# Performance work log

Hardware: AMD Instinct MI355X
Metric: run time of the kernel (lower is better)

Reference implementation:

```python
import math
import jax, jax.numpy as jnp
from jax import lax
import numpy as np

NUM_ANG_BINS = 8
NUM_SPATIAL_BINS = 4
SPATIAL_BIN_SIZE = 4
CLIPVAL = 0.2
STRIDE = 1
PAD = 1
EPS = 1e-10
DN = ('NCHW', 'OIHW', 'NCHW')


def _sift_pooling_kernel(ksize: int) -> np.ndarray:
    ks_2 = float(ksize) / 2.0
    xc2 = ks_2 - np.abs(np.arange(ksize, dtype=np.float32) + 0.5 - ks_2)
    return np.outer(xc2, xc2) / ks_2 ** 2  # (ksize, ksize)


def _reshape_kernel(kd: int, ky: int, kx: int) -> np.ndarray:
    numel = kd * ky * kx
    return np.eye(numel, dtype=np.float32).reshape(numel, kd, ky, kx)


def setup_inputs() -> dict:
    key = jax.random.key(0)
    x = jax.random.uniform(key, (2, 1, 512, 512), dtype=jnp.float32)
    pool_kernel = jnp.asarray(_sift_pooling_kernel(SPATIAL_BIN_SIZE))[None, None]  # (1,1,4,4)
    reshape_kernel = jnp.asarray(
        _reshape_kernel(NUM_ANG_BINS, NUM_SPATIAL_BINS, NUM_SPATIAL_BINS))  # (128,8,4,4)
    return {"x": x, "pool_kernel": pool_kernel, "reshape_kernel": reshape_kernel}


def _l2norm_c(t):
    # F.normalize(t, p=2, dim=1)
    n = jnp.sqrt(jnp.sum(t * t, axis=1, keepdims=True))
    return t / jnp.maximum(n, 1e-12)


def reference(x, pool_kernel, reshape_kernel):
    nbins = NUM_ANG_BINS
    two_pi = 2.0 * math.pi
    # spatial_gradient(mode='diff', normalized=True): central diff / 2 with replicate pad
    xp = jnp.pad(x, ((0, 0), (0, 0), (1, 1), (1, 1)), mode='edge')
    gx = 0.5 * (xp[:, :, 1:-1, 2:] - xp[:, :, 1:-1, :-2])
    gy = 0.5 * (xp[:, :, 2:, 1:-1] - xp[:, :, :-2, 1:-1])
    mag = jnp.sqrt(gx * gx + gy * gy + EPS)
    ori = jnp.arctan2(gy, gx + EPS) + two_pi
    o_big = nbins * ori / two_pi
    bo0f = jnp.floor(o_big)
    wo1 = o_big - bo0f
    bo0 = (bo0f.astype(jnp.int32) % nbins)[:, 0]          # (B,H,W)
    bo1 = (bo0 + 1) % nbins
    w0 = ((1.0 - wo1) * mag)[:, 0]                        # (B,H,W)
    w1 = (wo1 * mag)[:, 0]
    # soft-bin the magnitude into angular channels (vectorized over bins)
    ang = (jax.nn.one_hot(bo0, nbins, axis=1, dtype=x.dtype) * w0[:, None] +
           jax.nn.one_hot(bo1, nbins, axis=1, dtype=x.dtype) * w1[:, None])  # (B,8,H,W)
    # depthwise triangular pooling, padding ksize//2 -> (B,8,H+1,W+1)
    p = SPATIAL_BIN_SIZE // 2
    dw = jnp.tile(pool_kernel, (nbins, 1, 1, 1))  # (8,1,4,4)
    pooled = lax.conv_general_dilated(ang, dw, (1, 1), ((p, p), (p, p)),
                                      dimension_numbers=DN, feature_group_count=nbins)
    # neigh2channels identity conv -> (B,128,H,W)
    out = lax.conv_general_dilated(pooled, reshape_kernel, (STRIDE, STRIDE),
                                   ((PAD, PAD), (PAD, PAD)), dimension_numbers=DN)
    out = jnp.clip(_l2norm_c(out), 0.0, CLIPVAL)
    out = _l2norm_c(out)
    # RootSIFT
    n1 = jnp.maximum(jnp.sum(jnp.abs(out), axis=1, keepdims=True), 1e-12)
    out = jnp.sqrt(out / n1 + EPS)
    return out
```

## Files before the change

### kernel.cpp

```cpp
#include <hip/hip_runtime.h>
#include <hip/hip_fp16.h>
#include <math.h>

#define TY 4
#define TX 64
#define AH (TY + 6)
#define AW (TX + 6)
#define PH (TY + 3)
#define PW (TX + 3)
#define H 512
#define W 512

#define ANGX_OFF 0
#define ANG_OFF  21440
#define POOL_OFF 21440
#define SMEM_BYTES 36448

__device__ __forceinline__ unsigned short f2h(float f) {
    return __half_as_ushort(__float2half(f));
}
__device__ __forceinline__ float h2f_lo(unsigned int u) {
    return __half2float(__ushort_as_half((unsigned short)(u & 0xffffu)));
}
__device__ __forceinline__ float h2f_hi(unsigned int u) {
    return __half2float(__ushort_as_half((unsigned short)(u >> 16)));
}

__global__ __launch_bounds__(256, 4) void sift_kernel(const float* __restrict__ x,
                                                      float* __restrict__ out) {
    __shared__ __align__(16) char smem[SMEM_BYTES];
    float4* s_angx = (float4*)(smem + ANGX_OFF);
    uint4*  s_ang  = (uint4*)(smem + ANG_OFF);
    float4* s_pool = (float4*)(smem + POOL_OFF);

    const int tid = threadIdx.x;
    const int x0 = blockIdx.x * TX;
    const int y0 = blockIdx.y * TY;
    const int b  = blockIdx.z;
    const float* __restrict__ xb = x + (size_t)b * H * W;

    const float K1[4] = {0.25f, 0.75f, 0.75f, 0.25f};

    for (int i = tid; i < AH * AW; i += 256) {
        int ay = i / AW, ax = i - ay * AW;
        int gy = y0 - 3 + ay, gx = x0 - 3 + ax;
        float w0 = 0.f, w1 = 0.f;
        int bin = 0;
        if (gy >= 0 && gy < H && gx >= 0 && gx < W) {
            int gxm = gx - 1 < 0 ? 0 : gx - 1;
            int gxp = gx + 1 > W - 1 ? W - 1 : gx + 1;
            int gym = gy - 1 < 0 ? 0 : gy - 1;
            int gyp = gy + 1 > H - 1 ? H - 1 : gy + 1;
            float gxv = 0.5f * (xb[gy * W + gxp] - xb[gy * W + gxm]);
            float gyv = 0.5f * (xb[gyp * W + gx] - xb[gym * W + gx]);
            float mag = sqrtf(gxv * gxv + gyv * gyv + 1e-10f);
            float ori = atan2f(gyv, gxv + 1e-10f) + 6.283185307179586f;
            float obig = ori * 1.2732395447351628f;
            float bof = floorf(obig);
            float wo1 = obig - bof;
            bin = ((int)bof) & 7;
            w0 = (1.f - wo1) * mag;
            w1 = wo1 * mag;
        }
        unsigned short h0 = f2h(w0), h1 = f2h(w1);
        unsigned int pack01 = (unsigned int)h0 | ((unsigned int)h1 << 16);
        unsigned int ph0 = (unsigned int)h0 << 16;
        unsigned int pl1 = (unsigned int)h1;
        int j0 = bin >> 1;
        int j1 = ((bin + 1) & 7) >> 1;
        bool ev = (bin & 1) == 0;
        uint4 d;
        d.x = ev ? (j0 == 0 ? pack01 : 0u) : ((j0 == 0 ? ph0 : 0u) | (j1 == 0 ? pl1 : 0u));
        d.y = ev ? (j0 == 1 ? pack01 : 0u) : ((j0 == 1 ? ph0 : 0u) | (j1 == 1 ? pl1 : 0u));
        d.z = ev ? (j0 == 2 ? pack01 : 0u) : ((j0 == 2 ? ph0 : 0u) | (j1 == 2 ? pl1 : 0u));
        d.w = ev ? (j0 == 3 ? pack01 : 0u) : ((j0 == 3 ? ph0 : 0u) | (j1 == 3 ? pl1 : 0u));
        s_ang[i] = d;
    }
    __syncthreads();

    for (int i = tid; i < AH * PW; i += 256) {
        int ay = i / PW, pxl = i - ay * PW;
        float acc[8] = {0.f, 0.f, 0.f, 0.f, 0.f, 0.f, 0.f, 0.f};
        int base = ay * AW + pxl;
        #pragma unroll
        for (int v = 0; v < 4; ++v) {
            uint4 q = s_ang[base + v];
            float k = K1[v];
            acc[0] = fmaf(k, h2f_lo(q.x), acc[0]);
            acc[1] = fmaf(k, h2f_hi(q.x), acc[1]);
            acc[2] = fmaf(k, h2f_lo(q.y), acc[2]);
            acc[3] = fmaf(k, h2f_hi(q.y), acc[3]);
            acc[4] = fmaf(k, h2f_lo(q.z), acc[4]);
            acc[5] = fmaf(k, h2f_hi(q.z), acc[5]);
            acc[6] = fmaf(k, h2f_lo(q.w), acc[6]);
            acc[7] = fmaf(k, h2f_hi(q.w), acc[7]);
        }
        s_angx[(ay * 2 + 0) * PW + pxl] = make_float4(acc[0], acc[1], acc[2], acc[3]);
        s_angx[(ay * 2 + 1) * PW + pxl] = make_float4(acc[4], acc[5], acc[6], acc[7]);
    }
    __syncthreads();

    for (int i = tid; i < PH * PW * 2; i += 256) {
        int row = i / PW, pxl = i - row * PW;
        int pyl = row >> 1, dh = row & 1;
        float4 s = make_float4(0.f, 0.f, 0.f, 0.f);
        #pragma unroll
        for (int u = 0; u < 4; ++u) {
            float4 a = s_angx[((pyl + u) * 2 + dh) * PW + pxl];
            float k = K1[u];
            s.x = fmaf(k, a.x, s.x);
            s.y = fmaf(k, a.y, s.y);
            s.z = fmaf(k, a.z, s.z);
            s.w = fmaf(k, a.w, s.w);
        }
        bool valid = ((unsigned)(y0 - 1 + pyl) <= 512u) && ((unsigned)(x0 - 1 + pxl) <= 512u);
        if (!valid) s = make_float4(0.f, 0.f, 0.f, 0.f);
        s_pool[row * PW + pxl] = s;
    }
    __syncthreads();

    const int w  = tid >> 6;
    const int l  = tid & 63;
    const int dh = l >> 5;
    const int tx = 32 * (w & 1) + (l & 31);
    const int xx = x0 + tx;

    #pragma unroll
    for (int pp = 0; pp < 2; ++pp) {
        const int ty = 2 * pp + (w >> 1);
        const int yy = y0 + ty;
        float4 r[16];
        float ssq = 0.f;
        #pragma unroll
        for (int ky = 0; ky < 4; ++ky) {
            #pragma unroll
            for (int kx = 0; kx < 4; ++kx) {
                float4 t = s_pool[((ty + ky) * 2 + dh) * PW + (tx + kx)];
                r[ky * 4 + kx] = t;
                ssq = fmaf(t.x, t.x, ssq);
                ssq = fmaf(t.y, t.y, ssq);
                ssq = fmaf(t.z, t.z, ssq);
                ssq = fmaf(t.w, t.w, ssq);
            }
        }
        ssq += __shfl_xor(ssq, 32, 64);
        float inv = 1.f / fmaxf(sqrtf(ssq), 1e-12f);
        float su = 0.f;
        #pragma unroll
        for (int m = 0; m < 16; ++m) {
            float4 t = r[m];
            t.x = fminf(t.x * inv, 0.2f);
            t.y = fminf(t.y * inv, 0.2f);
            t.z = fminf(t.z * inv, 0.2f);
            t.w = fminf(t.w * inv, 0.2f);
            r[m] = t;
            su += (t.x + t.y) + (t.z + t.w);
        }
        su += __shfl_xor(su, 32, 64);
        float rs = 1.f / fmaxf(su, 1e-12f);
        float* __restrict__ op = out + ((size_t)b * 128 + dh * 64) * (size_t)(H * W)
                                     + (size_t)yy * W + xx;
        #pragma unroll
        for (int dd = 0; dd < 4; ++dd) {
            #pragma unroll
            for (int m = 0; m < 16; ++m) {
                float4 t = r[m];
                float comp = (dd == 0) ? t.x : (dd == 1) ? t.y : (dd == 2) ? t.z : t.w;
                float val = sqrtf(fmaf(comp, rs, 1e-10f));
                __builtin_nontemporal_store(val, op + (size_t)(dd * 16 + m) * (H * W));
            }
        }
    }
}

extern "C" void kernel_launch(void* const* d_in, const int* in_sizes, int n_in,
                              void* d_out, int out_size, void* d_ws, size_t ws_size,
                              hipStream_t stream) {
    const float* x = (const float*)d_in[0];
    float* out = (float*)d_out;
    const int B = in_sizes[0] / (H * W);
    dim3 grid(W / TX, H / TY, B);
    dim3 block(256);
    hipLaunchKernelGGL(sift_kernel, grid, block, 0, stream, x, out);
    (void)n_in; (void)out_size; (void)d_ws; (void)ws_size;
}
```

Before: 58.78 us.

## Compute two adjacent pixels per thread with 8-byte stores and fast math

Shared-memory pooled data is re-laid out as float2 per channel pair. Each thread now handles two horizontally adjacent pixels, reusing the overlapping 4x5 window, and writes float2 non-temporal stores. Per-pixel reductions now run across four lanes via shuffles. atan2 is replaced with a polynomial approximation that directly yields the bin coordinate, and sqrt, rcp and rsq use hardware intrinsics. This reduces store instruction count and transcendental cost, at the price of approximation error in orientation and normalization.

```diff
diff --git a/kernel.cpp b/kernel.cpp
--- a/kernel.cpp
+++ b/kernel.cpp
@@ -10,12 +10,15 @@
 #define PW (TX + 3)
 #define H 512
 #define W 512
+#define HW (H * W)
 
 #define ANGX_OFF 0
 #define ANG_OFF  21440
 #define POOL_OFF 21440
 #define SMEM_BYTES 36448
 
+typedef float f32x2 __attribute__((ext_vector_type(2)));
+
 __device__ __forceinline__ unsigned short f2h(float f) {
     return __half_as_ushort(__float2half(f));
 }
@@ -29,15 +32,16 @@
 __global__ __launch_bounds__(256, 4) void sift_kernel(const float* __restrict__ x,
                                                       float* __restrict__ out) {
     __shared__ __align__(16) char smem[SMEM_BYTES];
-    float4* s_angx = (float4*)(smem + ANGX_OFF);
-    uint4*  s_ang  = (uint4*)(smem + ANG_OFF);
-    float4* s_pool = (float4*)(smem + POOL_OFF);
+    float2* s_angx2 = (float2*)(smem + ANGX_OFF);
+    uint4*  s_ang   = (uint4*)(smem + ANG_OFF);
+    float2* s_pool2 = (float2*)(smem + POOL_OFF);
+    float*  s_poolf = (float*)(smem + POOL_OFF);
 
     const int tid = threadIdx.x;
     const int x0 = blockIdx.x * TX;
     const int y0 = blockIdx.y * TY;
     const int b  = blockIdx.z;
-    const float* __restrict__ xb = x + (size_t)b * H * W;
+    const float* __restrict__ xb = x + (size_t)b * HW;
 
     const float K1[4] = {0.25f, 0.75f, 0.75f, 0.25f};
 
@@ -48,17 +52,26 @@
         int bin = 0;
         if (gy >= 0 && gy < H && gx >= 0 && gx < W) {
             int gxm = gx - 1 < 0 ? 0 : gx - 1;
-            int gxp = gx + 1 > W - 1 ? W - 1 : gx + 1;
+            int gxp_ = gx + 1 > W - 1 ? W - 1 : gx + 1;
             int gym = gy - 1 < 0 ? 0 : gy - 1;
-            int gyp = gy + 1 > H - 1 ? H - 1 : gy + 1;
-            float gxv = 0.5f * (xb[gy * W + gxp] - xb[gy * W + gxm]);
-            float gyv = 0.5f * (xb[gyp * W + gx] - xb[gym * W + gx]);
-            float mag = sqrtf(gxv * gxv + gyv * gyv + 1e-10f);
-            float ori = atan2f(gyv, gxv + 1e-10f) + 6.283185307179586f;
-            float obig = ori * 1.2732395447351628f;
-            float bof = floorf(obig);
-            float wo1 = obig - bof;
-            bin = ((int)bof) & 7;
+            int gyp_ = gy + 1 > H - 1 ? H - 1 : gy + 1;
+            float gxv = 0.5f * (xb[gy * W + gxp_] - xb[gy * W + gxm]);
+            float gyv = 0.5f * (xb[gyp_ * W + gx] - xb[gym * W + gx]);
+            float mag = __builtin_amdgcn_sqrtf(gxv * gxv + gyv * gyv + 1e-10f);
+            float gxe = gxv + 1e-10f;
+            float axv = fabsf(gxe), ayv = fabsf(gyv);
+            float mn = fminf(axv, ayv), mx = fmaxf(axv, ayv);
+            float t = mn * __builtin_amdgcn_rcpf(fmaxf(mx, 1e-30f));
+            float t2 = t * t;
+            float p = t * fmaf(t2, fmaf(t2, fmaf(t2, fmaf(t2,
+                        fmaf(t2, -0.01492385f, 0.06704027f),
+                        -0.14824684f), 0.2464268f), -0.4235113f), 1.2732106f);
+            float q = (ayv > axv) ? (2.0f - p) : p;
+            q = (gxe < 0.0f) ? (4.0f - q) : q;
+            float o = (gyv < 0.0f) ? (0.0f - q) : q;
+            float of = floorf(o);
+            float wo1 = o - of;
+            bin = ((int)of) & 7;
             w0 = (1.f - wo1) * mag;
             w1 = wo1 * mag;
         }
@@ -95,79 +108,105 @@
             acc[6] = fmaf(k, h2f_lo(q.w), acc[6]);
             acc[7] = fmaf(k, h2f_hi(q.w), acc[7]);
         }
-        s_angx[(ay * 2 + 0) * PW + pxl] = make_float4(acc[0], acc[1], acc[2], acc[3]);
-        s_angx[(ay * 2 + 1) * PW + pxl] = make_float4(acc[4], acc[5], acc[6], acc[7]);
+        #pragma unroll
+        for (int g = 0; g < 4; ++g)
+            s_angx2[(ay * 4 + g) * PW + pxl] = make_float2(acc[2 * g], acc[2 * g + 1]);
     }
     __syncthreads();
 
-    for (int i = tid; i < PH * PW * 2; i += 256) {
+    for (int i = tid; i < PH * 4 * PW; i += 256) {
         int row = i / PW, pxl = i - row * PW;
-        int pyl = row >> 1, dh = row & 1;
-        float4 s = make_float4(0.f, 0.f, 0.f, 0.f);
+        int pyl = row >> 2, g = row & 3;
+        float2 s = make_float2(0.f, 0.f);
         #pragma unroll
         for (int u = 0; u < 4; ++u) {
-            float4 a = s_angx[((pyl + u) * 2 + dh) * PW + pxl];
+            float2 a = s_angx2[((pyl + u) * 4 + g) * PW + pxl];
             float k = K1[u];
             s.x = fmaf(k, a.x, s.x);
             s.y = fmaf(k, a.y, s.y);
-            s.z = fmaf(k, a.z, s.z);
-            s.w = fmaf(k, a.w, s.w);
         }
         bool valid = ((unsigned)(y0 - 1 + pyl) <= 512u) && ((unsigned)(x0 - 1 + pxl) <= 512u);
-        if (!valid) s = make_float4(0.f, 0.f, 0.f, 0.f);
-        s_pool[row * PW + pxl] = s;
+        if (!valid) s = make_float2(0.f, 0.f);
+        s_pool2[row * PW + pxl] = s;
     }
     __syncthreads();
 
-    const int w  = tid >> 6;
-    const int l  = tid & 63;
-    const int dh = l >> 5;
-    const int tx = 32 * (w & 1) + (l & 31);
-    const int xx = x0 + tx;
+    const int lane = tid & 63;
+    const int wv  = tid >> 6;
+    const int xq  = lane & 15;
+    const int g   = lane >> 4;
 
     #pragma unroll
-    for (int pp = 0; pp < 2; ++pp) {
-        const int ty = 2 * pp + (w >> 1);
-        const int yy = y0 + ty;
-        float4 r[16];
-        float ssq = 0.f;
+    for (int pass = 0; pass < 2; ++pass) {
+        const int hr  = wv * 2 + pass;
+        const int ty  = hr >> 1;
+        const int xh  = hr & 1;
+        const int txl = xh * 32 + 2 * xq;
+        const int yy  = y0 + ty;
+
+        float a[4][10];
+        #pragma unroll
+        for (int ky = 0; ky < 4; ++ky) {
+            const float* rp = s_poolf + (((ty + ky) * 4 + g) * PW + txl) * 2;
+            float4 q0 = *(const float4*)rp;
+            float4 q1 = *(const float4*)(rp + 4);
+            float2 q2 = *(const float2*)(rp + 8);
+            a[ky][0] = q0.x; a[ky][1] = q0.y; a[ky][2] = q0.z; a[ky][3] = q0.w;
+            a[ky][4] = q1.x; a[ky][5] = q1.y; a[ky][6] = q1.z; a[ky][7] = q1.w;
+            a[ky][8] = q2.x; a[ky][9] = q2.y;
+        }
+
+        float ssq0 = 0.f, ssq1 = 0.f;
         #pragma unroll
         for (int ky = 0; ky < 4; ++ky) {
             #pragma unroll
             for (int kx = 0; kx < 4; ++kx) {
-                float4 t = s_pool[((ty + ky) * 2 + dh) * PW + (tx + kx)];
-                r[ky * 4 + kx] = t;
-                ssq = fmaf(t.x, t.x, ssq);
-                ssq = fmaf(t.y, t.y, ssq);
-                ssq = fmaf(t.z, t.z, ssq);
-                ssq = fmaf(t.w, t.w, ssq);
+                float e0 = a[ky][2 * kx], e1 = a[ky][2 * kx + 1];
+                ssq0 = fmaf(e0, e0, ssq0); ssq0 = fmaf(e1, e1, ssq0);
+                float f0 = a[ky][2 * (kx + 1)], f1 = a[ky][2 * (kx + 1) + 1];
+                ssq1 = fmaf(f0, f0, ssq1); ssq1 = fmaf(f1, f1, ssq1);
             }
         }
-        ssq += __shfl_xor(ssq, 32, 64);
-        float inv = 1.f / fmaxf(sqrtf(ssq), 1e-12f);
-        float su = 0.f;
-        #pragma unroll
-        for (int m = 0; m < 16; ++m) {
-            float4 t = r[m];
-            t.x = fminf(t.x * inv, 0.2f);
-            t.y = fminf(t.y * inv, 0.2f);
-            t.z = fminf(t.z * inv, 0.2f);
-            t.w = fminf(t.w * inv, 0.2f);
-            r[m] = t;
-            su += (t.x + t.y) + (t.z + t.w);
-        }
-        su += __shfl_xor(su, 32, 64);
-        float rs = 1.f / fmaxf(su, 1e-12f);
-        float* __restrict__ op = out + ((size_t)b * 128 + dh * 64) * (size_t)(H * W)
-                                     + (size_t)yy * W + xx;
-        #pragma unroll
-        for (int dd = 0; dd < 4; ++dd) {
+        ssq0 += __shfl_xor(ssq0, 16, 64);
+        ssq0 += __shfl_xor(ssq0, 32, 64);
+        ssq1 += __shfl_xor(ssq1, 16, 64);
+        ssq1 += __shfl_xor(ssq1, 32, 64);
+        float inv0 = __builtin_amdgcn_rsqf(fmaxf(ssq0, 1e-24f));
+        float inv1 = __builtin_amdgcn_rsqf(fmaxf(ssq1, 1e-24f));
+
+        float su0 = 0.f, su1 = 0.f;
+        #pragma unroll
+        for (int ky = 0; ky < 4; ++ky) {
             #pragma unroll
-            for (int m = 0; m < 16; ++m) {
-                float4 t = r[m];
-                float comp = (dd == 0) ? t.x : (dd == 1) ? t.y : (dd == 2) ? t.z : t.w;
-                float val = sqrtf(fmaf(comp, rs, 1e-10f));
-                __builtin_nontemporal_store(val, op + (size_t)(dd * 16 + m) * (H * W));
+            for (int kx = 0; kx < 4; ++kx) {
+                su0 += fminf(a[ky][2 * kx] * inv0, 0.2f)
+                     + fminf(a[ky][2 * kx + 1] * inv0, 0.2f);
+                su1 += fminf(a[ky][2 * (kx + 1)] * inv1, 0.2f)
+                     + fminf(a[ky][2 * (kx + 1) + 1] * inv1, 0.2f);
+            }
+        }
+        su0 += __shfl_xor(su0, 16, 64);
+        su0 += __shfl_xor(su0, 32, 64);
+        su1 += __shfl_xor(su1, 16, 64);
+        su1 += __shfl_xor(su1, 32, 64);
+        float rs0 = __builtin_amdgcn_rcpf(fmaxf(su0, 1e-12f));
+        float rs1 = __builtin_amdgcn_rcpf(fmaxf(su1, 1e-12f));
+
+        #pragma unroll
+        for (int s = 0; s < 2; ++s) {
+            float* __restrict__ bp = out + ((size_t)b * 128 + (size_t)((2 * g + s) * 16)) * HW
+                                         + (size_t)yy * W + (x0 + txl);
+            #pragma unroll
+            for (int ky = 0; ky < 4; ++ky) {
+                #pragma unroll
+                for (int kx = 0; kx < 4; ++kx) {
+                    float u0 = fminf(a[ky][2 * kx + s] * inv0, 0.2f);
+                    float u1 = fminf(a[ky][2 * (kx + 1) + s] * inv1, 0.2f);
+                    f32x2 val;
+                    val.x = __builtin_amdgcn_sqrtf(fmaf(u0, rs0, 1e-10f));
+                    val.y = __builtin_amdgcn_sqrtf(fmaf(u1, rs1, 1e-10f));
+                    __builtin_nontemporal_store(val, (f32x2*)(bp + (size_t)(ky * 4 + kx) * HW));
+                }
             }
         }
     }
```

Result: slower. 63.00 us (+7.2%).
